# Kernel tuning notes

Hardware: AMD Instinct MI355X
Metric: run time of the kernel (lower is better)

## Reference

```python
import jax, jax.numpy as jnp
import numpy as np

B, H, W = 12, 192, 640
EPS = 1e-7
THRESHOLD = 0.98


def _normalize_flow(f):
    # torch: 2*(f - min)/(max - min) - 1 with GLOBAL min/max
    mn = f.min()
    mx = f.max()
    return 2.0 * (f - mn) / (mx - mn) - 1.0


def setup_inputs() -> dict:
    key = jax.random.key(0)
    ks = jax.random.split(key, 4)
    # optical flow in pixels (up to ~tens of px displacement)
    flow = jax.random.normal(ks[0], (B, 2, H, W), jnp.float32) * 20.0
    depth = jax.random.uniform(ks[1], (B, 1, H, W), jnp.float32, minval=0.1, maxval=10.0)
    # realistic pinhole intrinsics (KITTI-like), padded to 4x4
    Kn = np.eye(4, dtype=np.float32)
    Kn[0, 0] = 0.58 * W
    Kn[1, 1] = 1.92 * H
    Kn[0, 2] = 0.5 * W
    Kn[1, 2] = 0.5 * H
    K = jnp.tile(jnp.asarray(Kn)[None], (B, 1, 1))
    invK = jnp.tile(jnp.asarray(np.linalg.inv(Kn))[None], (B, 1, 1))
    # small-motion camera pose: identity rotation + small translation
    t = jax.random.normal(ks[2], (B, 3), jnp.float32) * 0.05
    pose = jnp.tile(jnp.eye(4, dtype=jnp.float32)[None], (B, 1, 1)).at[:, :3, 3].set(t)
    segmentation = jax.random.randint(ks[3], (B, 1, H, W), 0, 2) > 0
    return {"flow": flow, "depth": depth, "K": K, "invK": invK,
            "pose": pose, "segmentation": segmentation}


def reference(flow, depth, K, invK, pose, segmentation):
    gx = jnp.arange(W, dtype=jnp.float32)
    gy = jnp.arange(H, dtype=jnp.float32)
    grid = jnp.stack(jnp.meshgrid(gx, gy, indexing='xy'), axis=0)  # [2,H,W]

    # ---- compute_dynamic_flow: BackprojectDepth + Project3D + normalize + mask ----
    flow_n = _normalize_flow(flow)
    pix = jnp.concatenate([grid.reshape(2, -1),
                           jnp.ones((1, H * W), jnp.float32)], axis=0)  # [3,HW]
    cam = jnp.einsum('bij,jn->bin', invK[:, :3, :3], pix)               # [B,3,HW]
    cam = depth.reshape(B, 1, -1) * cam
    points = jnp.concatenate([cam, jnp.ones((B, 1, H * W), cam.dtype)], axis=1)  # [B,4,HW]
    P = jnp.matmul(K, pose)[:, :3, :]                                   # [B,3,4]
    cp = jnp.einsum('bij,bjn->bin', P, points)                          # [B,3,HW]
    pix_locs = (cp[:, :2] / (cp[:, 2:3] + EPS)).reshape(B, 2, H, W)
    static_n = _normalize_flow(pix_locs - grid[None])
    dyn = flow_n - static_n
    check = jnp.sqrt(jnp.sum(dyn * dyn, axis=1, keepdims=True))         # [B,1,H,W]
    check = (check - check.min()) / (check.max() - check.min())
    motion_mask = check < THRESHOLD

    coords = jnp.round(grid[None] + flow).astype(jnp.int32)             # [B,2,H,W]
    cxi = jnp.clip(coords[:, 0], 0, W - 1)
    cyi = jnp.clip(coords[:, 1], 0, H - 1)
    idx = (cyi * W + cxi).reshape(B, -1)                                # [B,HW]

    def scat(idx_b, vals_b):  # vals_b: [C,HW] -> scatter columns to idx_b
        return jnp.zeros_like(vals_b).at[:, idx_b].set(vals_b)

    bwd_flow = jax.vmap(scat)(idx, (-flow).reshape(B, 2, -1)).reshape(B, 2, H, W)
    seg_ref = jax.vmap(scat)(idx, segmentation.reshape(B, 1, -1)).reshape(B, 1, H, W)

    return motion_mask, bwd_flow, seg_ref
```

## Files before the change

### kernel.cpp

```cpp
#include <hip/hip_runtime.h>
#include <math.h>

#pragma clang fp contract(off)

namespace {

constexpr int B = 12, H = 192, W = 640;
constexpr int HW  = H * W;
constexpr int BHW = B * HW;
constexpr float EPS = 1e-7f;

constexpr int TR    = 24;
constexpr int TILES = H / TR;
constexpr int TRW   = TR * W;
constexpr int SC    = 4;
constexpr int HWC   = HW / SC;
constexpr int NBLK  = B * TILES * SC;
constexpr int SPB   = HW / (TILES * SC);
constexpr int WTPB  = 1024;
constexpr int RBLK  = 256;
constexpr int RTPB  = 1024;


__device__ __forceinline__ void computeP(const float* __restrict__ Kb,
                                         const float* __restrict__ Po, float* P) {
#pragma unroll
    for (int i = 0; i < 3; ++i)
#pragma unroll
        for (int j = 0; j < 4; ++j) {
            float s = Kb[i*4+0] * Po[0*4+j];
            s = s + Kb[i*4+1] * Po[1*4+j];
            s = s + Kb[i*4+2] * Po[2*4+j];
            s = s + Kb[i*4+3] * Po[3*4+j];
            P[i*4+j] = s;
        }
}

__device__ __forceinline__ void static_flow_P(
    const float* __restrict__ iK, const float* __restrict__ P,
    int x, int y, float d, float& sx, float& sy)
{
    float fx = (float)x, fy = (float)y;
    float cam0 = iK[0]*fx + iK[1]*fy + iK[2];
    float cam1 = iK[4]*fx + iK[5]*fy + iK[6];
    float cam2 = iK[8]*fx + iK[9]*fy + iK[10];
    cam0 = d * cam0; cam1 = d * cam1; cam2 = d * cam2;
    float cp0 = P[0]*cam0 + P[1]*cam1 + P[2]*cam2  + P[3];
    float cp1 = P[4]*cam0 + P[5]*cam1 + P[6]*cam2  + P[7];
    float cp2 = P[8]*cam0 + P[9]*cam1 + P[10]*cam2 + P[11];
    float pz = cp2 + EPS;
    sx = cp0 / pz - fx;
    sy = cp1 / pz - fy;
}

__device__ __forceinline__ float norm01(float v, float mn, float mx) {
    return (2.0f * (v - mn)) / (mx - mn) - 1.0f;
}

__device__ __forceinline__ void blockRed4(float& a0, float& a1, float& a2, float& a3,
                                          float (*sred)[4], float* bc) {
    for (int off = 32; off; off >>= 1) {
        a0 = fminf(a0, __shfl_down(a0, off, 64));
        a1 = fmaxf(a1, __shfl_down(a1, off, 64));
        a2 = fminf(a2, __shfl_down(a2, off, 64));
        a3 = fmaxf(a3, __shfl_down(a3, off, 64));
    }
    int lane = threadIdx.x & 63, wv = threadIdx.x >> 6;
    if (lane == 0) { sred[wv][0]=a0; sred[wv][1]=a1; sred[wv][2]=a2; sred[wv][3]=a3; }
    __syncthreads();
    if (threadIdx.x == 0) {
#pragma unroll
        for (int w = 1; w < 16; ++w) {
            a0 = fminf(a0, sred[w][0]); a1 = fmaxf(a1, sred[w][1]);
            a2 = fminf(a2, sred[w][2]); a3 = fmaxf(a3, sred[w][3]);
        }
        bc[0]=a0; bc[1]=a1; bc[2]=a2; bc[3]=a3;
    }
    __syncthreads();
    a0=bc[0]; a1=bc[1]; a2=bc[2]; a3=bc[3];
}

__device__ __forceinline__ void blockRed2(float& a0, float& a1,
                                          float (*sred)[4], float* bc) {
    for (int off = 32; off; off >>= 1) {
        a0 = fminf(a0, __shfl_down(a0, off, 64));
        a1 = fmaxf(a1, __shfl_down(a1, off, 64));
    }
    int lane = threadIdx.x & 63, wv = threadIdx.x >> 6;
    if (lane == 0) { sred[wv][0]=a0; sred[wv][1]=a1; }
    __syncthreads();
    if (threadIdx.x == 0) {
#pragma unroll
        for (int w = 1; w < 16; ++w) {
            a0 = fminf(a0, sred[w][0]); a1 = fmaxf(a1, sred[w][1]);
        }
        bc[0]=a0; bc[1]=a1;
    }
    __syncthreads();
    a0=bc[0]; a1=bc[1];
}

__global__ void __launch_bounds__(WTPB, 8)
k_winner(const float* __restrict__ flow, const float* __restrict__ depth,
         const float* __restrict__ Km, const float* __restrict__ invK,
         const float* __restrict__ pose,
         unsigned short* __restrict__ partial, float* __restrict__ redA) {
    __shared__ unsigned int win[TRW];
    __shared__ float sred[16][4];
    __shared__ float bc[4];

    const int wg    = blockIdx.x;
    const int chunk = wg & (SC - 1);
    const int bt    = wg >> 2;
    const int b     = bt / TILES;
    const int tile  = bt - b * TILES;
    const int t0    = tile * TR;

    const float* fx_p = flow + b * 2 * HW;
    const float* fy_p = fx_p + HW;

    for (int i = threadIdx.x; i < TRW; i += WTPB) win[i] = 0u;
    __syncthreads();

    float fmn = INFINITY, fmx = -INFINITY, smn = INFINITY, smx = -INFINITY;
    const int s_beg = chunk * HWC;
    const int s_end = s_beg + HWC;
    for (int s0 = s_beg + threadIdx.x * 4; s0 < s_end; s0 += WTPB * 4) {
        float4 fx4 = *(const float4*)(fx_p + s0);
        float4 fy4 = *(const float4*)(fy_p + s0);
        fmn = fminf(fmn, fminf(fminf(fx4.x, fx4.y), fminf(fx4.z, fx4.w)));
        fmx = fmaxf(fmx, fmaxf(fmaxf(fx4.x, fx4.y), fmaxf(fx4.z, fx4.w)));
        fmn = fminf(fmn, fminf(fminf(fy4.x, fy4.y), fminf(fy4.z, fy4.w)));
        fmx = fmaxf(fmx, fmaxf(fmaxf(fy4.x, fy4.y), fmaxf(fy4.z, fy4.w)));
        int y = s0 / W;
        int x = s0 - y * W;
        float fxa[4] = {fx4.x, fx4.y, fx4.z, fx4.w};
        float fya[4] = {fy4.x, fy4.y, fy4.z, fy4.w};
#pragma unroll
        for (int j = 0; j < 4; ++j) {
            int cxi = (int)rintf((float)(x + j) + fxa[j]);
            int cyi = (int)rintf((float)y + fya[j]);
            cxi = min(max(cxi, 0), W - 1);
            cyi = min(max(cyi, 0), H - 1);
            if (cyi >= t0 && cyi < t0 + TR) {
                unsigned key = (unsigned)(s0 + j + 1 - s_beg);
                atomicMax(&win[(cyi - t0) * W + cxi], key);
            }
        }
    }
    __syncthreads();
    {
        unsigned short* dst = partial + (size_t)wg * TRW;
        for (int i = threadIdx.x; i < TRW; i += WTPB)
            dst[i] = (unsigned short)win[i];
    }

    {
        const float* iK = invK + b * 16;
        float P[12];
        computeP(Km + b * 16, pose + b * 16, P);
        int n0s = chunk * HWC + tile * SPB;
        if (threadIdx.x < SPB / 4) {
            int n = n0s + threadIdx.x * 4;
            int y = n / W;
            int x0 = n - y * W;
            float4 d4 = *(const float4*)(depth + b * HW + n);
            float da[4] = {d4.x, d4.y, d4.z, d4.w};
#pragma unroll
            for (int j = 0; j < 4; ++j) {
                float sx, sy;
                static_flow_P(iK, P, x0 + j, y, da[j], sx, sy);
                smn = fminf(smn, fminf(sx, sy));
                smx = fmaxf(smx, fmaxf(sx, sy));
            }
        }
    }
    blockRed4(fmn, fmx, smn, smx, sred, bc);
    if (threadIdx.x == 0) {
        redA[wg*4+0] = fmn; redA[wg*4+1] = fmx;
        redA[wg*4+2] = smn; redA[wg*4+3] = smx;
    }
}

__global__ void __launch_bounds__(RTPB)
k_red2(const float* __restrict__ flow, const float* __restrict__ depth,
       const float* __restrict__ Km, const float* __restrict__ invK,
       const float* __restrict__ pose,
       const float* __restrict__ redA, float* __restrict__ redB,
       float* __restrict__ out) {
    __shared__ float sred[16][4];
    __shared__ float bc[4];

    float gfmn = INFINITY, gfmx = -INFINITY, gsmn = INFINITY, gsmx = -INFINITY;
    for (int i = threadIdx.x; i < NBLK; i += RTPB) {
        gfmn = fminf(gfmn, redA[i*4+0]); gfmx = fmaxf(gfmx, redA[i*4+1]);
        gsmn = fminf(gsmn, redA[i*4+2]); gsmx = fmaxf(gsmx, redA[i*4+3]);
    }
    blockRed4(gfmn, gfmx, gsmn, gsmx, sred, bc);

    float cmn = INFINITY, cmx = -INFINITY;
    int bCur = -1;
    float P[12];
    int stride = gridDim.x * blockDim.x;
    for (int g = blockIdx.x * blockDim.x + threadIdx.x; g < BHW / 4; g += stride) {
        int p0 = g * 4;
        int b  = p0 / HW;
        if (b != bCur) { computeP(Km + b * 16, pose + b * 16, P); bCur = b; }
        const float* iK = invK + b * 16;
        int n0 = p0 - b * HW;
        int y  = n0 / W;
        int x0 = n0 - y * W;
        float4 fx4 = *(const float4*)(flow + b*2*HW + n0);
        float4 fy4 = *(const float4*)(flow + b*2*HW + HW + n0);
        float4 d4  = *(const float4*)(depth + p0);
        float fxa[4] = {fx4.x, fx4.y, fx4.z, fx4.w};
        float fya[4] = {fy4.x, fy4.y, fy4.z, fy4.w};
        float da[4]  = {d4.x, d4.y, d4.z, d4.w};
        float4 cv;
        float* cva = (float*)&cv;
#pragma unroll
        for (int j = 0; j < 4; ++j) {
            float sx, sy;
            static_flow_P(iK, P, x0 + j, y, da[j], sx, sy);
            float dx = norm01(fxa[j], gfmn, gfmx) - norm01(sx, gsmn, gsmx);
            float dy = norm01(fya[j], gfmn, gfmx) - norm01(sy, gsmn, gsmx);
            float c = sqrtf(dx*dx + dy*dy);
            cva[j] = c;
            cmn = fminf(cmn, c); cmx = fmaxf(cmx, c);
        }
        *(float4*)(out + p0) = cv;
    }
    blockRed2(cmn, cmx, sred, bc);
    if (threadIdx.x == 0) { redB[blockIdx.x*2] = cmn; redB[blockIdx.x*2+1] = cmx; }
}

__global__ void __launch_bounds__(RTPB)
k_mask(const float* __restrict__ flow, const int* __restrict__ seg,
       const float* __restrict__ redB, const unsigned short* __restrict__ partial,
       float* __restrict__ out) {
    __shared__ float sred[16][4];
    __shared__ float bc[4];

    float gcmn = INFINITY, gcmx = -INFINITY;
    for (int i = threadIdx.x; i < RBLK; i += RTPB) {
        gcmn = fminf(gcmn, redB[2*i]); gcmx = fmaxf(gcmx, redB[2*i+1]);
    }
    blockRed2(gcmn, gcmx, sred, bc);

    int stride = gridDim.x * blockDim.x;
    for (int p = blockIdx.x * blockDim.x + threadIdx.x; p < BHW; p += stride) {
        float c  = out[p];
        float cn = (c - gcmn) / (gcmx - gcmn);
        out[p] = (cn < 0.98f) ? 1.0f : 0.0f;

        int b    = p / HW;
        int n    = p - b * HW;
        int tile = n / TRW;
        int off  = n - tile * TRW;
        const unsigned short* base =
            partial + (size_t)(b * TILES + tile) * SC * TRW + off;
        int nw = -1;
#pragma unroll
        for (int cch = 0; cch < SC; ++cch) {
            unsigned k = base[(size_t)cch * TRW];
            if (k) nw = cch * HWC + (int)k - 1;
        }
        float bx = 0.0f, by = 0.0f, sg = 0.0f;
        if (nw >= 0) {
            bx = -flow[b*2*HW + nw];
            by = -flow[b*2*HW + HW + nw];
            sg = seg[b*HW + nw] ? 1.0f : 0.0f;
        }
        out[BHW + b*2*HW + n]      = bx;
        out[BHW + b*2*HW + HW + n] = by;
        out[3*BHW + p]             = sg;
    }
}

}

extern "C" void kernel_launch(void* const* d_in, const int* in_sizes, int n_in,
                              void* d_out, int out_size, void* d_ws, size_t ws_size,
                              hipStream_t stream) {
    const float* flow  = (const float*)d_in[0];
    const float* depth = (const float*)d_in[1];
    const float* Km    = (const float*)d_in[2];
    const float* invK  = (const float*)d_in[3];
    const float* pose  = (const float*)d_in[4];
    const int*   seg   = (const int*)d_in[5];
    float* out = (float*)d_out;

    float* redA = (float*)d_ws;
    float* redB = (float*)((char*)d_ws + 8192);
    unsigned short* partial = (unsigned short*)((char*)d_ws + 16384);

    k_winner<<<NBLK, WTPB, 0, stream>>>(flow, depth, Km, invK, pose, partial, redA);
    k_red2  <<<RBLK, RTPB, 0, stream>>>(flow, depth, Km, invK, pose, redA, redB, out);
    k_mask  <<<RBLK, RTPB, 0, stream>>>(flow, seg, redB, partial, out);
}
```

Before: 139.3 us.

## Fuse reduction and mask kernels using a software grid barrier

Merges the second reduction kernel and the mask/scatter-gather kernel into one persistent kernel. Blocks publish their partial min/max, increment a global counter reset in the first kernel, then do the backward-flow gather while other blocks finish, and spin-wait before thresholding. This removes one kernel launch and overlaps the barrier wait with independent gather work. The cost is a spin barrier that relies on all 256 blocks being resident at once, which deadlocks if they are not.

```diff
diff --git a/kernel.cpp b/kernel.cpp
--- a/kernel.cpp
+++ b/kernel.cpp
@@ -18,8 +18,9 @@
 constexpr int NBLK  = B * TILES * SC;
 constexpr int SPB   = HW / (TILES * SC);
 constexpr int WTPB  = 1024;
-constexpr int RBLK  = 256;
-constexpr int RTPB  = 1024;
+
+constexpr int FBLK  = 256;
+constexpr int FTPB  = 1024;
 
 
 __device__ __forceinline__ void computeP(const float* __restrict__ Kb,
@@ -104,7 +105,9 @@
 k_winner(const float* __restrict__ flow, const float* __restrict__ depth,
          const float* __restrict__ Km, const float* __restrict__ invK,
          const float* __restrict__ pose,
-         unsigned short* __restrict__ partial, float* __restrict__ redA) {
+         unsigned short* __restrict__ partial, float* __restrict__ redA,
+         unsigned int* __restrict__ bar) {
+    if (blockIdx.x == 0 && threadIdx.x == 0) *bar = 0u;
     __shared__ unsigned int win[TRW];
     __shared__ float sred[16][4];
     __shared__ float bc[4];
@@ -182,17 +185,19 @@
     }
 }
 
-__global__ void __launch_bounds__(RTPB)
-k_red2(const float* __restrict__ flow, const float* __restrict__ depth,
-       const float* __restrict__ Km, const float* __restrict__ invK,
-       const float* __restrict__ pose,
-       const float* __restrict__ redA, float* __restrict__ redB,
-       float* __restrict__ out) {
+__global__ void __launch_bounds__(FTPB, 4)
+k_final(const float* __restrict__ flow, const float* __restrict__ depth,
+        const int* __restrict__ seg,
+        const float* __restrict__ Km, const float* __restrict__ invK,
+        const float* __restrict__ pose,
+        const float* __restrict__ redA, float* __restrict__ redB,
+        const unsigned short* __restrict__ partial,
+        unsigned int* __restrict__ bar, float* __restrict__ out) {
     __shared__ float sred[16][4];
     __shared__ float bc[4];
 
     float gfmn = INFINITY, gfmx = -INFINITY, gsmn = INFINITY, gsmx = -INFINITY;
-    for (int i = threadIdx.x; i < NBLK; i += RTPB) {
+    for (int i = threadIdx.x; i < NBLK; i += FTPB) {
         gfmn = fminf(gfmn, redA[i*4+0]); gfmx = fmaxf(gfmx, redA[i*4+1]);
         gsmn = fminf(gsmn, redA[i*4+2]); gsmx = fmaxf(gsmx, redA[i*4+3]);
     }
@@ -201,7 +206,7 @@
     float cmn = INFINITY, cmx = -INFINITY;
     int bCur = -1;
     float P[12];
-    int stride = gridDim.x * blockDim.x;
+    const int stride = FBLK * FTPB;
     for (int g = blockIdx.x * blockDim.x + threadIdx.x; g < BHW / 4; g += stride) {
         int p0 = g * 4;
         int b  = p0 / HW;
@@ -231,28 +236,16 @@
         *(float4*)(out + p0) = cv;
     }
     blockRed2(cmn, cmx, sred, bc);
-    if (threadIdx.x == 0) { redB[blockIdx.x*2] = cmn; redB[blockIdx.x*2+1] = cmx; }
-}
-
-__global__ void __launch_bounds__(RTPB)
-k_mask(const float* __restrict__ flow, const int* __restrict__ seg,
-       const float* __restrict__ redB, const unsigned short* __restrict__ partial,
-       float* __restrict__ out) {
-    __shared__ float sred[16][4];
-    __shared__ float bc[4];
-
-    float gcmn = INFINITY, gcmx = -INFINITY;
-    for (int i = threadIdx.x; i < RBLK; i += RTPB) {
-        gcmn = fminf(gcmn, redB[2*i]); gcmx = fmaxf(gcmx, redB[2*i+1]);
-    }
-    blockRed2(gcmn, gcmx, sred, bc);
-
-    int stride = gridDim.x * blockDim.x;
+    if (threadIdx.x == 0) {
+        __hip_atomic_store(&redB[blockIdx.x*2],   cmn, __ATOMIC_RELAXED,
+                           __HIP_MEMORY_SCOPE_AGENT);
+        __hip_atomic_store(&redB[blockIdx.x*2+1], cmx, __ATOMIC_RELAXED,
+                           __HIP_MEMORY_SCOPE_AGENT);
+        __threadfence();
+        atomicAdd(bar, 1u);
+    }
+
     for (int p = blockIdx.x * blockDim.x + threadIdx.x; p < BHW; p += stride) {
-        float c  = out[p];
-        float cn = (c - gcmn) / (gcmx - gcmn);
-        out[p] = (cn < 0.98f) ? 1.0f : 0.0f;
-
         int b    = p / HW;
         int n    = p - b * HW;
         int tile = n / TRW;
@@ -274,6 +267,28 @@
         out[BHW + b*2*HW + n]      = bx;
         out[BHW + b*2*HW + HW + n] = by;
         out[3*BHW + p]             = sg;
+    }
+
+    if (threadIdx.x == 0) {
+        while (__hip_atomic_load(bar, __ATOMIC_ACQUIRE,
+                                 __HIP_MEMORY_SCOPE_AGENT) < (unsigned)FBLK)
+            __builtin_amdgcn_s_sleep(1);
+    }
+    __syncthreads();
+
+    float gcmn = INFINITY, gcmx = -INFINITY;
+    if (threadIdx.x < FBLK) {
+        gcmn = __hip_atomic_load(&redB[threadIdx.x*2],   __ATOMIC_RELAXED,
+                                 __HIP_MEMORY_SCOPE_AGENT);
+        gcmx = __hip_atomic_load(&redB[threadIdx.x*2+1], __ATOMIC_RELAXED,
+                                 __HIP_MEMORY_SCOPE_AGENT);
+    }
+    blockRed2(gcmn, gcmx, sred, bc);
+
+    for (int p = blockIdx.x * blockDim.x + threadIdx.x; p < BHW; p += stride) {
+        float c  = out[p];
+        float cn = (c - gcmn) / (gcmx - gcmn);
+        out[p] = (cn < 0.98f) ? 1.0f : 0.0f;
     }
 }
 
@@ -292,9 +307,11 @@
 
     float* redA = (float*)d_ws;
     float* redB = (float*)((char*)d_ws + 8192);
+    unsigned int* bar = (unsigned int*)((char*)d_ws + 12288);
     unsigned short* partial = (unsigned short*)((char*)d_ws + 16384);
 
-    k_winner<<<NBLK, WTPB, 0, stream>>>(flow, depth, Km, invK, pose, partial, redA);
-    k_red2  <<<RBLK, RTPB, 0, stream>>>(flow, depth, Km, invK, pose, redA, redB, out);
-    k_mask  <<<RBLK, RTPB, 0, stream>>>(flow, seg, redB, partial, out);
-}
+    k_winner<<<NBLK, WTPB, 0, stream>>>(flow, depth, Km, invK, pose,
+                                        partial, redA, bar);
+    k_final <<<FBLK, FTPB, 0, stream>>>(flow, depth, seg, Km, invK, pose,
+                                        redA, redB, partial, bar, out);
+}
```

New measurement: 145.6 us. 4.6% more time.
